# Performance work log

Hardware: AMD Instinct MI355X
Metric: run time of the kernel (lower is better)

Reference implementation:

```python
import jax, jax.numpy as jnp
import numpy as np

B, S, D, H = 8, 1024, 1024, 16
DH = D // H


def setup_inputs() -> dict:
    key = jax.random.key(0)
    ks = jax.random.split(key, 8)
    en = jax.random.normal(ks[0], (B, S, D), dtype=jnp.float32)
    fr = jax.random.normal(ks[1], (B, S, D), dtype=jnp.float32)
    l_en = jax.random.randint(ks[2], (B,), 1, S + 1)
    l_fr = jax.random.randint(ks[3], (B,), 1, S + 1)
    # nn.Linear-style params (weight stored [out, in])
    lim_q = 1.0 / np.sqrt(D)
    W_Q_w = jax.random.uniform(ks[4], (D, D), minval=-lim_q, maxval=lim_q, dtype=jnp.float32)
    W_Q_b = jax.random.uniform(ks[5], (D,), minval=-lim_q, maxval=lim_q, dtype=jnp.float32)
    W_KV_w = jax.random.uniform(ks[6], (2 * D, D), minval=-lim_q, maxval=lim_q, dtype=jnp.float32)
    W_KV_b = jax.random.uniform(ks[7], (2 * D,), minval=-lim_q, maxval=lim_q, dtype=jnp.float32)
    return {"en": en, "fr": fr, "l_en": l_en, "l_fr": l_fr,
            "W_Q_w": W_Q_w, "W_Q_b": W_Q_b, "W_KV_w": W_KV_w, "W_KV_b": W_KV_b}


def reference(en, fr, l_en, l_fr, W_Q_w, W_Q_b, W_KV_w, W_KV_b):
    # q from decoder (fr), k/v from encoder (en)
    q = (fr @ W_Q_w.T + W_Q_b).reshape(B, S, H, DH).transpose(0, 2, 1, 3)  # [B,H,S,DH]
    kv = (en @ W_KV_w.T + W_KV_b).reshape(B, S, 2, H, DH).transpose(2, 0, 3, 1, 4)
    k, v = kv[0], kv[1]  # [B,H,S,DH]

    # NOTE: original scales by sqrt(embedding_dim), not sqrt(head_dim)
    attn = jnp.einsum('bhqd,bhkd->bhqk', q, k) / jnp.sqrt(jnp.float32(D))

    pos = jnp.arange(S)
    mask_en = (pos[None, :] < l_en[:, None])  # [B,S] key mask
    mask_fr = (pos[None, :] < l_fr[:, None])  # [B,S] query mask
    mask = (mask_fr[:, :, None] & mask_en[:, None, :])[:, None, :, :]  # [B,1,Sq,Sk]

    attn = jnp.where(mask, attn, -jnp.inf)
    attn = jax.nn.softmax(attn, axis=-1)
    attn = jnp.nan_to_num(attn)  # fully-masked rows -> 0 (matches torch nan_to_num)

    out = jnp.einsum('bhqk,bhkd->bhqd', attn, v)  # [B,H,S,DH]
    return out.transpose(0, 2, 1, 3).reshape(B, S, D)
```

## Files before the change

### kernel.cpp

```cpp
#include <hip/hip_runtime.h>
#include <hip/hip_bf16.h>
#include <stdint.h>

typedef __bf16 bf16_t;
typedef bf16_t bf16x8 __attribute__((ext_vector_type(8)));
typedef float f32x4 __attribute__((ext_vector_type(4)));
typedef unsigned short ushortx8 __attribute__((ext_vector_type(8)));

__device__ __forceinline__ uint16_t f2bf(float f) {
  uint32_t u = __float_as_uint(f);
  uint32_t r = u + 0x7FFFu + ((u >> 16) & 1u);
  return (uint16_t)(r >> 16);
}

__device__ __forceinline__ int read_len(const int* __restrict__ p, int b) {
  bool is64 = (p[1] == 0) | (p[3] == 0) | (p[5] == 0) | (p[7] == 0);
  return is64 ? p[2 * b] : p[b];
}

#define GLDS16(gp, lp)                                                   \
  __builtin_amdgcn_global_load_lds(                                      \
      (const __attribute__((address_space(1))) uint32_t*)(gp),           \
      (__attribute__((address_space(3))) uint32_t*)(lp), 16, 0, 0)

__global__ void cvt4_kernel(const float* __restrict__ s0, uint16_t* __restrict__ d0, int n0,
                            const float* __restrict__ s1, uint16_t* __restrict__ d1, int n1,
                            const float* __restrict__ s2, uint16_t* __restrict__ d2, int n2,
                            const float* __restrict__ s3, uint16_t* __restrict__ d3, int n3,
                            const int* __restrict__ msk2, const int* __restrict__ msk3) {
  int e = (blockIdx.x * blockDim.x + threadIdx.x) * 4;
  const float* s;
  uint16_t* d;
  const int* msk = nullptr;
  if (e < n0) { s = s0 + e; d = d0 + e; }
  else if ((e -= n0) < n1) { s = s1 + e; d = d1 + e; }
  else if ((e -= n1) < n2) { s = s2 + e; d = d2 + e; msk = msk2; }
  else if ((e -= n2) < n3) { s = s3 + e; d = d3 + e; msk = msk3; }
  else return;
  if (msk) {
    int row = (e >> 10) & 1023, b = e >> 20;
    int need = (read_len(msk, b) + 127) & ~127;
    if (row >= need) return;
  }
  const float4 v = *reinterpret_cast<const float4*>(s);
  ushort4 o;
  o.x = f2bf(v.x); o.y = f2bf(v.y); o.z = f2bf(v.z); o.w = f2bf(v.w);
  *reinterpret_cast<ushort4*>(d) = o;
}

__global__ __launch_bounds__(512) void gemm_fast(
    const uint16_t* __restrict__ frB, const uint16_t* __restrict__ enB,
    const uint16_t* __restrict__ wq, const uint16_t* __restrict__ wkv,
    const float* __restrict__ bq, const float* __restrict__ bkv,
    const int* __restrict__ l_en_p, const int* __restrict__ l_fr_p,
    uint16_t* __restrict__ Qb,
    uint16_t* __restrict__ Kb,
    uint16_t* __restrict__ Vb) {
  __shared__ __attribute__((aligned(16))) uint16_t As[3][128 * 64];
  __shared__ __attribute__((aligned(16))) uint16_t Bs[2][128 * 64];
  const int t = threadIdx.x;
  const int lane = t & 63;
  const int w = t >> 6;
  const int wm = w >> 2, wn = w & 3;
  const int l15 = lane & 15, lg = lane >> 4;

  const int orig = blockIdx.x;
  const int xcd = orig & 7;
  const int slot = orig >> 3;
  const bool isQ = slot < 64;
  int b, bn;
  if (isQ) { b = slot >> 3; bn = (slot & 7) * 128; }
  else { int s2 = slot - 64; b = s2 >> 4; bn = (s2 & 15) * 128; }
  const int i = (xcd - b) & 7;
  const int bm = b * 1024 + i * 128;

  const int need = isQ ? read_len(l_fr_p, b) : read_len(l_en_p, b);
  if (i * 128 >= need) return;

  const uint16_t* Bw = isQ ? wq : wkv;
  const float* bias = isQ ? bq : bkv;
  const float scale = isQ ? 0.03125f : 1.0f;
  const uint16_t* Ab = isQ ? frB : enB;

  f32x4 acc[4][2];
#pragma unroll
  for (int ii = 0; ii < 4; ++ii)
#pragma unroll
    for (int j = 0; j < 2; ++j) acc[ii][j] = (f32x4){0.f, 0.f, 0.f, 0.f};

  auto stageB = [&](int buf, int kt) {
#pragma unroll
    for (int ii = 0; ii < 2; ++ii) {
      int g = t + 512 * ii;
      int L = g ^ ((g >> 3) & 7);
      int row = L >> 3, k8 = L & 7;
      GLDS16(Bw + (size_t)(bn + row) * 1024 + kt + k8 * 8, &Bs[buf][g * 8]);
    }
  };
  auto stageA = [&](int buf, int kt) {
#pragma unroll
    for (int ii = 0; ii < 2; ++ii) {
      int g = t + 512 * ii;
      int L = g ^ ((g >> 3) & 7);
      int row = L >> 3, k8 = L & 7;
      GLDS16(Ab + (size_t)(bm + row) * 1024 + kt + k8 * 8, &As[buf][g * 8]);
    }
  };
  auto computeAB = [&](int bufA, int bufB) {
#pragma unroll
    for (int ks = 0; ks < 2; ++ks) {
      const int kb = ks * 64 + lg * 16;
      bf16x8 af[4], bf[2];
#pragma unroll
      for (int mf = 0; mf < 4; ++mf) {
        int row = wm * 64 + mf * 16 + l15;
        int byte = (row * 128 + kb) ^ ((row & 7) << 4);
        af[mf] = *reinterpret_cast<const bf16x8*>(
            reinterpret_cast<const char*>(As[bufA]) + byte);
      }
#pragma unroll
      for (int nf = 0; nf < 2; ++nf) {
        int row = wn * 32 + nf * 16 + l15;
        int byte = (row * 128 + kb) ^ ((row & 7) << 4);
        bf[nf] = *reinterpret_cast<const bf16x8*>(
            reinterpret_cast<const char*>(Bs[bufB]) + byte);
      }
#pragma unroll
      for (int mf = 0; mf < 4; ++mf)
#pragma unroll
        for (int nf = 0; nf < 2; ++nf)
          acc[mf][nf] = __builtin_amdgcn_mfma_f32_16x16x32_bf16(
              af[mf], bf[nf], acc[mf][nf], 0, 0, 0);
    }
  };

  stageA(0, 0);
  stageB(0, 0);
  stageA(1, 64);
  asm volatile("s_waitcnt vmcnt(2)" ::: "memory");
  __builtin_amdgcn_s_barrier();
  __builtin_amdgcn_sched_barrier(0);
  int aC = 0, bC = 0;
  for (int tt = 0; tt < 16; ++tt) {
    if (tt + 1 < 16) stageB(bC ^ 1, (tt + 1) * 64);
    if (tt + 2 < 16) stageA(aC >= 1 ? aC - 1 : aC + 2, (tt + 2) * 64);
    computeAB(aC, bC);
    if (tt < 15) {
      if (tt < 14) asm volatile("s_waitcnt vmcnt(2)" ::: "memory");
      else         asm volatile("s_waitcnt vmcnt(0)" ::: "memory");
      __builtin_amdgcn_s_barrier();
      __builtin_amdgcn_sched_barrier(0);
    }
    aC = (aC == 2) ? 0 : aC + 1;
    bC ^= 1;
  }

#pragma unroll
  for (int mf = 0; mf < 4; ++mf) {
#pragma unroll
    for (int nf = 0; nf < 2; ++nf) {
      int n = bn + wn * 32 + nf * 16 + l15;
      float bv = bias[n];
#pragma unroll
      for (int r = 0; r < 4; ++r) {
        int m = bm + wm * 64 + mf * 16 + lg * 4 + r;
        float v = (acc[mf][nf][r] + bv) * scale;
        uint16_t o = f2bf(v);
        int bb = m >> 10, s = m & 1023;
        if (isQ) {
          int h = n >> 6, d = n & 63;
          Qb[((((bb * 16 + h) << 10) | s) << 6) | d] = o;
        } else if (n < 1024) {
          int h = n >> 6, d = n & 63;
          Kb[((((bb * 16 + h) << 10) | s) << 6) | d] = o;
        } else {
          int n2 = n - 1024;
          int h = n2 >> 6, d = n2 & 63;
          Vb[((((bb * 16 + h) << 6) | d) << 10) | s] = o;
        }
      }
    }
  }
}

__global__ __launch_bounds__(256) void gemm_fb(
    const float* __restrict__ frF, const float* __restrict__ enF,
    const uint16_t* __restrict__ wq, const uint16_t* __restrict__ wkv,
    const float* __restrict__ bq, const float* __restrict__ bkv,
    const int* __restrict__ l_en_p, const int* __restrict__ l_fr_p,
    uint16_t* __restrict__ Qb, uint16_t* __restrict__ Kb,
    uint16_t* __restrict__ Vb) {
  __shared__ __attribute__((aligned(16))) uint16_t As[2][128 * 64];
  __shared__ __attribute__((aligned(16))) uint16_t Bs[2][128 * 64];
  const int t = threadIdx.x;
  const int lane = t & 63;
  const int w = t >> 6;
  const int wm = w >> 1, wn = w & 1;
  const int l15 = lane & 15, lg = lane >> 4;

  const int orig = blockIdx.x;
  const int xcd = orig & 7;
  const int slot = orig >> 3;
  const bool isQ = slot < 64;
  int b, bn;
  if (isQ) { b = slot >> 3; bn = (slot & 7) * 128; }
  else { int s2 = slot - 64; b = s2 >> 4; bn = (s2 & 15) * 128; }
  const int i = (xcd - b) & 7;
  const int bm = b * 1024 + i * 128;

  const int need = isQ ? read_len(l_fr_p, b) : read_len(l_en_p, b);
  if (i * 128 >= need) return;

  const uint16_t* Bw = isQ ? wq : wkv;
  const float* bias = isQ ? bq : bkv;
  const float scale = isQ ? 0.03125f : 1.0f;
  const float* Af = isQ ? frF : enF;

  f32x4 acc[4][4];
#pragma unroll
  for (int ii = 0; ii < 4; ++ii)
#pragma unroll
    for (int j = 0; j < 4; ++j) acc[ii][j] = (f32x4){0.f, 0.f, 0.f, 0.f};

  float4 ar0[4], ar1[4];

  auto stageB = [&](int buf, int kt) {
#pragma unroll
    for (int ii = 0; ii < 4; ++ii) {
      int g = t + 256 * ii;
      int L = g ^ ((g >> 3) & 7);
      int row = L >> 3, k8 = L & 7;
      GLDS16(Bw + (size_t)(bn + row) * 1024 + kt + k8 * 8, &Bs[buf][g * 8]);
    }
  };
  auto loadA_f32 = [&](int kt) {
#pragma unroll
    for (int ii = 0; ii < 4; ++ii) {
      int L = t + 256 * ii;
      int row = L >> 3, k8 = L & 7;
      const float* src = Af + (size_t)(bm + row) * 1024 + kt + k8 * 8;
      ar0[ii] = *reinterpret_cast<const float4*>(src);
      ar1[ii] = *reinterpret_cast<const float4*>(src + 4);
    }
  };
  auto writeA = [&](int buf) {
#pragma unroll
    for (int ii = 0; ii < 4; ++ii) {
      int L = t + 256 * ii;
      int row = L >> 3, k8 = L & 7;
      ushortx8 o;
      o[0] = f2bf(ar0[ii].x); o[1] = f2bf(ar0[ii].y);
      o[2] = f2bf(ar0[ii].z); o[3] = f2bf(ar0[ii].w);
      o[4] = f2bf(ar1[ii].x); o[5] = f2bf(ar1[ii].y);
      o[6] = f2bf(ar1[ii].z); o[7] = f2bf(ar1[ii].w);
      int byte = (row * 128 + k8 * 16) ^ ((row & 7) << 4);
      *reinterpret_cast<ushortx8*>(reinterpret_cast<char*>(As[buf]) + byte) = o;
    }
  };
  auto compute = [&](int buf) {
#pragma unroll
    for (int ks = 0; ks < 2; ++ks) {
      const int kb = ks * 64 + lg * 16;
      bf16x8 af[4], bf[4];
#pragma unroll
      for (int mf = 0; mf < 4; ++mf) {
        int row = wm * 64 + mf * 16 + l15;
        int byte = (row * 128 + kb) ^ ((row & 7) << 4);
        af[mf] = *reinterpret_cast<const bf16x8*>(
            reinterpret_cast<const char*>(As[buf]) + byte);
      }
#pragma unroll
      for (int nf = 0; nf < 4; ++nf) {
        int row = wn * 64 + nf * 16 + l15;
        int byte = (row * 128 + kb) ^ ((row & 7) << 4);
        bf[nf] = *reinterpret_cast<const bf16x8*>(
            reinterpret_cast<const char*>(Bs[buf]) + byte);
      }
#pragma unroll
      for (int mf = 0; mf < 4; ++mf)
#pragma unroll
        for (int nf = 0; nf < 4; ++nf)
          acc[mf][nf] = __builtin_amdgcn_mfma_f32_16x16x32_bf16(
              af[mf], bf[nf], acc[mf][nf], 0, 0, 0);
    }
  };
  loadA_f32(0);
  stageB(0, 0);
  writeA(0);
  __syncthreads();
#pragma unroll 2
  for (int tt = 0; tt < 16; ++tt) {
    const int cur = tt & 1;
    const int ktn = (tt + 1) * 64;
    if (tt < 15) { stageB(cur ^ 1, ktn); loadA_f32(ktn); }
    compute(cur);
    if (tt < 15) writeA(cur ^ 1);
    __syncthreads();
  }

#pragma unroll
  for (int mf = 0; mf < 4; ++mf) {
#pragma unroll
    for (int nf = 0; nf < 4; ++nf) {
      int n = bn + wn * 64 + nf * 16 + l15;
      float bv = bias[n];
#pragma unroll
      for (int r = 0; r < 4; ++r) {
        int m = bm + wm * 64 + mf * 16 + lg * 4 + r;
        float v = (acc[mf][nf][r] + bv) * scale;
        uint16_t o = f2bf(v);
        int bb = m >> 10, s = m & 1023;
        if (isQ) {
          int h = n >> 6, d = n & 63;
          Qb[((((bb * 16 + h) << 10) | s) << 6) | d] = o;
        } else if (n < 1024) {
          int h = n >> 6, d = n & 63;
          Kb[((((bb * 16 + h) << 10) | s) << 6) | d] = o;
        } else {
          int n2 = n - 1024;
          int h = n2 >> 6, d = n2 & 63;
          Vb[((((bb * 16 + h) << 6) | d) << 10) | s] = o;
        }
      }
    }
  }
}

__global__ __launch_bounds__(512) void attn_kernel(
    const uint16_t* __restrict__ Qb,
    const uint16_t* __restrict__ Kb,
    const uint16_t* __restrict__ Vt,
    const int* __restrict__ l_en_p, const int* __restrict__ l_fr_p,
    float* __restrict__ out) {
  __shared__ __attribute__((aligned(16))) uint16_t Ks[2][64 * 64];
  __shared__ __attribute__((aligned(16))) uint16_t Vs[2][64 * 64];
  __shared__ __attribute__((aligned(16))) bf16_t Ps[8][16][72];
  const int t = threadIdx.x;
  const int lane = t & 63, w = t >> 6;
  const int l15 = lane & 15, lg = lane >> 4;
  const int orig = blockIdx.x;
  const int xcd = orig & 7;
  const int slot = orig >> 3;
  const int b = slot >> 4;
  const int rest = slot & 15;
  const int h = xcd + 8 * (rest >> 3);
  const int q0 = (rest & 7) << 7;
  const int bh = b * 16 + h;
  const int len_en = read_len(l_en_p, b);
  const int len_fr = read_len(l_fr_p, b);

  if (q0 >= len_fr) {
    for (int i = t; i < 128 * 64; i += 512) {
      int rr = i >> 6, cc = i & 63;
      out[(size_t)(b * 1024 + q0 + rr) * 1024 + h * 64 + cc] = 0.f;
    }
    return;
  }

  const uint16_t* qbase =
      Qb + ((size_t)bh * 1024 + q0 + w * 16 + l15) * 64 + lg * 8;
  const bf16x8 aq0 = *reinterpret_cast<const bf16x8*>(qbase);
  const bf16x8 aq1 = *reinterpret_cast<const bf16x8*>(qbase + 32);

  float mrow[4], lrow[4];
  f32x4 oacc[4];
#pragma unroll
  for (int r = 0; r < 4; ++r) { mrow[r] = -1e30f; lrow[r] = 0.f; }
#pragma unroll
  for (int df = 0; df < 4; ++df) oacc[df] = (f32x4){0.f, 0.f, 0.f, 0.f};

  auto stage = [&](int buf, int j0) {
    int g = t;
    int L = g ^ ((g >> 3) & 7);
    int row = L >> 3, k8 = L & 7;
    GLDS16(Kb + ((size_t)bh * 1024 + j0 + row) * 64 + k8 * 8, &Ks[buf][g * 8]);
    GLDS16(Vt + ((size_t)bh * 64 + row) * 1024 + j0 + k8 * 8, &Vs[buf][g * 8]);
  };

  const int ntiles = (len_en + 63) >> 6;
  stage(0, 0);
  __syncthreads();

  for (int tt = 0; tt < ntiles; ++tt) {
    const int cur = tt & 1;
    const int j0 = tt * 64;
    if (tt + 1 < ntiles) stage(cur ^ 1, (tt + 1) * 64);

    f32x4 sc[4];
#pragma unroll
    for (int nf = 0; nf < 4; ++nf) sc[nf] = (f32x4){0.f, 0.f, 0.f, 0.f};
    __builtin_amdgcn_s_setprio(1);
#pragma unroll
    for (int ks = 0; ks < 2; ++ks) {
      const bf16x8 aq = ks ? aq1 : aq0;
      const int kb = ks * 64 + lg * 16;
#pragma unroll
      for (int nf = 0; nf < 4; ++nf) {
        int row = nf * 16 + l15;
        int byte = (row * 128 + kb) ^ ((row & 7) << 4);
        bf16x8 bk = *reinterpret_cast<const bf16x8*>(
            reinterpret_cast<const char*>(Ks[cur]) + byte);
        sc[nf] = __builtin_amdgcn_mfma_f32_16x16x32_bf16(aq, bk, sc[nf], 0, 0, 0);
      }
    }
    __builtin_amdgcn_s_setprio(0);
#pragma unroll
    for (int nf = 0; nf < 4; ++nf) {
      int col = j0 + nf * 16 + l15;
      if (col >= len_en) sc[nf] = (f32x4){-1e30f, -1e30f, -1e30f, -1e30f};
    }
    float tm[4];
#pragma unroll
    for (int r = 0; r < 4; ++r)
      tm[r] = fmaxf(fmaxf(sc[0][r], sc[1][r]), fmaxf(sc[2][r], sc[3][r]));
#pragma unroll
    for (int off = 1; off < 16; off <<= 1)
#pragma unroll
      for (int r = 0; r < 4; ++r) tm[r] = fmaxf(tm[r], __shfl_xor(tm[r], off));

    bool small = (tm[0] <= mrow[0] + 8.f) && (tm[1] <= mrow[1] + 8.f) &&
                 (tm[2] <= mrow[2] + 8.f) && (tm[3] <= mrow[3] + 8.f);
    if (!__all(small)) {
      float fac[4];
#pragma unroll
      for (int r = 0; r < 4; ++r) {
        float mn = fmaxf(mrow[r], tm[r]);
        fac[r] = __expf(mrow[r] - mn);
        mrow[r] = mn;
      }
#pragma unroll
      for (int r = 0; r < 4; ++r) lrow[r] *= fac[r];
#pragma unroll
      for (int df = 0; df < 4; ++df)
#pragma unroll
        for (int r = 0; r < 4; ++r) oacc[df][r] *= fac[r];
    }
    float ps[4] = {0.f, 0.f, 0.f, 0.f};
#pragma unroll
    for (int nf = 0; nf < 4; ++nf)
#pragma unroll
      for (int r = 0; r < 4; ++r) {
        float p = __expf(sc[nf][r] - mrow[r]);
        ps[r] += p;
        Ps[w][lg * 4 + r][nf * 16 + l15] = (bf16_t)p;
      }
#pragma unroll
    for (int off = 1; off < 16; off <<= 1)
#pragma unroll
      for (int r = 0; r < 4; ++r) ps[r] += __shfl_xor(ps[r], off);
#pragma unroll
    for (int r = 0; r < 4; ++r) lrow[r] += ps[r];

    __builtin_amdgcn_s_setprio(1);
#pragma unroll
    for (int ks = 0; ks < 2; ++ks) {
      const bf16x8 pa = *reinterpret_cast<const bf16x8*>(
          &Ps[w][l15][0] + ks * 32 + lg * 8);
#pragma unroll
      for (int df = 0; df < 4; ++df) {
        int row = df * 16 + l15;
        int byte = (row * 128 + ks * 64 + lg * 16) ^ ((row & 7) << 4);
        bf16x8 bv = *reinterpret_cast<const bf16x8*>(
            reinterpret_cast<const char*>(Vs[cur]) + byte);
        oacc[df] = __builtin_amdgcn_mfma_f32_16x16x32_bf16(pa, bv, oacc[df], 0, 0, 0);
      }
    }
    __builtin_amdgcn_s_setprio(0);
    __syncthreads();
  }

#pragma unroll
  for (int df = 0; df < 4; ++df)
#pragma unroll
    for (int r = 0; r < 4; ++r) {
      int q = q0 + w * 16 + lg * 4 + r;
      float inv = (q < len_fr && lrow[r] > 0.f) ? 1.0f / lrow[r] : 0.f;
      out[(size_t)(b * 1024 + q) * 1024 + h * 64 + df * 16 + l15] =
          oacc[df][r] * inv;
    }
}

extern "C" void kernel_launch(void* const* d_in, const int* in_sizes, int n_in,
                              void* d_out, int out_size, void* d_ws,
                              size_t ws_size, hipStream_t stream) {
  const float* en = (const float*)d_in[0];
  const float* fr = (const float*)d_in[1];
  const int* l_en = (const int*)d_in[2];
  const int* l_fr = (const int*)d_in[3];
  const float* wq = (const float*)d_in[4];
  const float* bq = (const float*)d_in[5];
  const float* wkv = (const float*)d_in[6];
  const float* bkv = (const float*)d_in[7];
  float* out = (float*)d_out;

  char* ws = (char*)d_ws;
  uint16_t* wq_bf = (uint16_t*)(ws);
  uint16_t* wkv_bf = (uint16_t*)(ws + 2097152);
  uint16_t* Qbuf = (uint16_t*)(ws + 6291456);
  uint16_t* Kbuf = (uint16_t*)(ws + 23068672);
  uint16_t* Vtbuf = (uint16_t*)(ws + 39845888);
  uint16_t* fr_bf = (uint16_t*)(ws + 56623104);
  uint16_t* en_bf = (uint16_t*)(ws + 73400320);
  const bool pre = ws_size >= 90177536ull;

  if (pre) {
    cvt4_kernel<<<19456, 256, 0, stream>>>(wq, wq_bf, 1048576,
                                           wkv, wkv_bf, 2097152,
                                           fr, fr_bf, 8388608,
                                           en, en_bf, 8388608,
                                           l_fr, l_en);
    gemm_fast<<<1536, 512, 0, stream>>>(fr_bf, en_bf, wq_bf, wkv_bf, bq, bkv,
                                        l_en, l_fr, Qbuf, Kbuf, Vtbuf);
  } else {
    cvt4_kernel<<<3072, 256, 0, stream>>>(wq, wq_bf, 1048576,
                                          wkv, wkv_bf, 2097152,
                                          nullptr, nullptr, 0,
                                          nullptr, nullptr, 0,
                                          nullptr, nullptr);
    gemm_fb<<<1536, 256, 0, stream>>>(fr, en, wq_bf, wkv_bf, bq, bkv,
                                      l_en, l_fr, Qbuf, Kbuf, Vtbuf);
  }

  attn_kernel<<<1024, 512, 0, stream>>>(Qbuf, Kbuf, Vtbuf, l_en, l_fr, out);
}
```

Before: 113.9 us.

## Triple-buffer attention K/V tiles with vmcnt waits; widen conversion kernel to 8 elements

The attention loop moves from double to triple buffering of K/V tiles. It prefetches two tiles ahead and replaces the full __syncthreads with an explicit s_waitcnt vmcnt plus s_barrier, so loads stay in flight across iterations. The fp32-to-bf16 conversion kernel now handles 8 elements per thread, and its argument order is changed so the masked activations come first. The cost is more LDS per block, and the hand-written vmcnt counts depend on exactly two loads per stage.

```diff
diff --git a/kernel.cpp b/kernel.cpp
--- a/kernel.cpp
+++ b/kernel.cpp
@@ -27,25 +27,27 @@
                             const float* __restrict__ s1, uint16_t* __restrict__ d1, int n1,
                             const float* __restrict__ s2, uint16_t* __restrict__ d2, int n2,
                             const float* __restrict__ s3, uint16_t* __restrict__ d3, int n3,
-                            const int* __restrict__ msk2, const int* __restrict__ msk3) {
-  int e = (blockIdx.x * blockDim.x + threadIdx.x) * 4;
+                            const int* __restrict__ msk0, const int* __restrict__ msk1) {
+  int e = (blockIdx.x * blockDim.x + threadIdx.x) * 8;
   const float* s;
   uint16_t* d;
   const int* msk = nullptr;
-  if (e < n0) { s = s0 + e; d = d0 + e; }
-  else if ((e -= n0) < n1) { s = s1 + e; d = d1 + e; }
-  else if ((e -= n1) < n2) { s = s2 + e; d = d2 + e; msk = msk2; }
-  else if ((e -= n2) < n3) { s = s3 + e; d = d3 + e; msk = msk3; }
+  if (e < n0) { s = s0 + e; d = d0 + e; msk = msk0; }
+  else if ((e -= n0) < n1) { s = s1 + e; d = d1 + e; msk = msk1; }
+  else if ((e -= n1) < n2) { s = s2 + e; d = d2 + e; }
+  else if ((e -= n2) < n3) { s = s3 + e; d = d3 + e; }
   else return;
   if (msk) {
     int row = (e >> 10) & 1023, b = e >> 20;
     int need = (read_len(msk, b) + 127) & ~127;
     if (row >= need) return;
   }
-  const float4 v = *reinterpret_cast<const float4*>(s);
-  ushort4 o;
-  o.x = f2bf(v.x); o.y = f2bf(v.y); o.z = f2bf(v.z); o.w = f2bf(v.w);
-  *reinterpret_cast<ushort4*>(d) = o;
+  const float4 v0 = *reinterpret_cast<const float4*>(s);
+  const float4 v1 = *reinterpret_cast<const float4*>(s + 4);
+  ushortx8 o;
+  o[0] = f2bf(v0.x); o[1] = f2bf(v0.y); o[2] = f2bf(v0.z); o[3] = f2bf(v0.w);
+  o[4] = f2bf(v1.x); o[5] = f2bf(v1.y); o[6] = f2bf(v1.z); o[7] = f2bf(v1.w);
+  *reinterpret_cast<ushortx8*>(d) = o;
 }
 
 __global__ __launch_bounds__(512) void gemm_fast(
@@ -332,8 +334,8 @@
     const uint16_t* __restrict__ Vt,
     const int* __restrict__ l_en_p, const int* __restrict__ l_fr_p,
     float* __restrict__ out) {
-  __shared__ __attribute__((aligned(16))) uint16_t Ks[2][64 * 64];
-  __shared__ __attribute__((aligned(16))) uint16_t Vs[2][64 * 64];
+  __shared__ __attribute__((aligned(16))) uint16_t Ks[3][64 * 64];
+  __shared__ __attribute__((aligned(16))) uint16_t Vs[3][64 * 64];
   __shared__ __attribute__((aligned(16))) bf16_t Ps[8][16][72];
   const int t = threadIdx.x;
   const int lane = t & 63, w = t >> 6;
@@ -379,12 +381,19 @@
 
   const int ntiles = (len_en + 63) >> 6;
   stage(0, 0);
-  __syncthreads();
-
+  if (ntiles > 1) {
+    stage(1, 64);
+    asm volatile("s_waitcnt vmcnt(2)" ::: "memory");
+  } else {
+    asm volatile("s_waitcnt vmcnt(0)" ::: "memory");
+  }
+  __builtin_amdgcn_s_barrier();
+  __builtin_amdgcn_sched_barrier(0);
+
+  int cur = 0;
   for (int tt = 0; tt < ntiles; ++tt) {
-    const int cur = tt & 1;
     const int j0 = tt * 64;
-    if (tt + 1 < ntiles) stage(cur ^ 1, (tt + 1) * 64);
+    if (tt + 2 < ntiles) stage(cur >= 1 ? cur - 1 : 2, (tt + 2) * 64);
 
     f32x4 sc[4];
 #pragma unroll
@@ -466,7 +475,14 @@
       }
     }
     __builtin_amdgcn_s_setprio(0);
-    __syncthreads();
+
+    if (tt + 1 < ntiles) {
+      if (tt + 2 < ntiles) asm volatile("s_waitcnt vmcnt(2)" ::: "memory");
+      else                 asm volatile("s_waitcnt vmcnt(0)" ::: "memory");
+      __builtin_amdgcn_s_barrier();
+      __builtin_amdgcn_sched_barrier(0);
+    }
+    cur = (cur == 2) ? 0 : cur + 1;
   }
 
 #pragma unroll
@@ -504,15 +520,15 @@
   const bool pre = ws_size >= 90177536ull;
 
   if (pre) {
-    cvt4_kernel<<<19456, 256, 0, stream>>>(wq, wq_bf, 1048576,
-                                           wkv, wkv_bf, 2097152,
-                                           fr, fr_bf, 8388608,
-                                           en, en_bf, 8388608,
-                                           l_fr, l_en);
+    cvt4_kernel<<<9728, 256, 0, stream>>>(fr, fr_bf, 8388608,
+                                          en, en_bf, 8388608,
+                                          wq, wq_bf, 1048576,
+                                          wkv, wkv_bf, 2097152,
+                                          l_fr, l_en);
     gemm_fast<<<1536, 512, 0, stream>>>(fr_bf, en_bf, wq_bf, wkv_bf, bq, bkv,
                                         l_en, l_fr, Qbuf, Kbuf, Vtbuf);
   } else {
-    cvt4_kernel<<<3072, 256, 0, stream>>>(wq, wq_bf, 1048576,
+    cvt4_kernel<<<1536, 256, 0, stream>>>(wq, wq_bf, 1048576,
                                           wkv, wkv_bf, 2097152,
                                           nullptr, nullptr, 0,
                                           nullptr, nullptr, 0,
```

Measured after the change: 108.2 us (median of 2 runs). 5.0% less time.
